# Optimization experiments

Measured on AMD Instinct MI355X. Metric: run time of the kernel, lower is better.

Reference implementation:

```python
import jax, jax.numpy as jnp
import numpy as np

B, SEQ, NVAR, DM, K = 2, 512, 64, 128, 2
SCALE = DM ** -0.5  # ScaledDotProductAttention scale, lsa=False so constant


def _period_branch(x4, Wel, bel, Wq, bq, Wk, bk, Wv, bv, Wo, bo, period):
    # x4: [B, DM(time), NVAR, DM(dim)] -- output of start_embed
    pad = (-DM) % period
    pn = (DM + pad) // period  # period_num
    xp = jnp.pad(x4, ((0, 0), (0, pad), (0, 0), (0, 0)))
    # torch .unfold(dim=1, size=period, step=period) -> [B, pn, NVAR, DM, period]
    xw = xp.reshape(B, pn, period, NVAR, DM).transpose(0, 1, 3, 4, 2)
    # emb_linear over the d_model (dim) axis
    xw = jnp.einsum('bqndl,ed->bqnel', xw, Wel) + bel[None, None, None, :, None]
    # -> [B, NVAR, dim, pn, period] then flatten to conv1d layout [bn, dim, L]
    X = xw.transpose(0, 2, 3, 1, 4).reshape(B * NVAR, DM, pn * period)
    # 1x1 Conv1d QKV projections over the channel (dim) axis
    q = jnp.einsum('bdl,ed->bel', X, Wq) + bq[None, :, None]
    k = jnp.einsum('bdl,ed->bel', X, Wk) + bk[None, :, None]
    v = jnp.einsum('bdl,ed->bel', X, Wv) + bv[None, :, None]
    q_s = q.reshape(B * NVAR, DM, pn, period).transpose(0, 1, 3, 2)  # [bn,dim,pl,pn]
    k_s = k.reshape(B * NVAR, DM, pn, period)                         # [bn,dim,pn,pl]
    v_s = v.reshape(B * NVAR, DM, pn, period).transpose(0, 1, 3, 2)  # [bn,dim,pl,pn]
    attn = jax.nn.softmax(jnp.einsum('bdip,bdpj->bdij', q_s, k_s) * SCALE, axis=-1)
    o = jnp.einsum('bdij,bdjp->bdip', attn, v_s)  # [bn, dim, period, pn]
    o = o.reshape(B * NVAR, DM, period * pn)[:, :, :DM]  # truncate to n_heads=DM
    return o @ Wo.T + bo  # to_out Linear(n_heads, n_heads), dropout eval-mode


def reference(x, W_emb, b_emb, W_start, b_start, Wel, bel, Wq, bq, Wk, bk, Wv, bv, Wo, bo, f1, f2):
    # inverted embedding: Linear(seq_len->d_model) over time, then permute -> [B, DM, NVAR]
    xe = (jnp.einsum('bsn,sd->bnd', x, W_emb) + b_emb).transpose(0, 2, 1)
    # FFT_for_Period amplitudes; top-k frequency indices f1,f2 are static (host-side in torch)
    amp = jnp.abs(jnp.fft.rfft(xe, axis=1)).mean(-1)  # [B, DM//2+1]
    pw = jax.nn.softmax(jnp.stack([amp[:, f1], amp[:, f2]], -1), axis=-1)  # [B, K]
    # start_embed: Linear(1 -> d_model) -> [B, DM, NVAR, DM]
    x4 = xe[..., None] * W_start + b_start
    outs = [_period_branch(x4, Wel, bel, Wq, bq, Wk, bk, Wv, bv, Wo, bo, DM // f)
            for f in (f1, f2)]
    res = jnp.stack(outs, -1)                      # [B*NVAR, DM, DM, K]
    pw_b = jnp.repeat(pw, NVAR, axis=0)            # [B*NVAR, K] (b-major order matches reshape)
    out = (res * pw_b[:, None, None, :]).sum(-1)
    return out.reshape(B, NVAR, DM, DM)


def setup_inputs() -> dict:
    key = jax.random.key(0)
    ks = jax.random.split(key, 16)
    s = 0.02
    d = {
        'x': jax.random.normal(ks[0], (B, SEQ, NVAR), jnp.float32),
        'W_emb': jax.random.normal(ks[1], (SEQ, DM), jnp.float32) * s,
        'b_emb': jax.random.normal(ks[2], (DM,), jnp.float32) * s,
        'W_start': jax.random.normal(ks[3], (DM,), jnp.float32) * s,
        'b_start': jax.random.normal(ks[4], (DM,), jnp.float32) * s,
        'Wel': jax.random.normal(ks[5], (DM, DM), jnp.float32) * s,
        'bel': jax.random.normal(ks[6], (DM,), jnp.float32) * s,
        'Wq': jax.random.normal(ks[7], (DM, DM), jnp.float32) * s,
        'bq': jax.random.normal(ks[8], (DM,), jnp.float32) * s,
        'Wk': jax.random.normal(ks[9], (DM, DM), jnp.float32) * s,
        'bk': jax.random.normal(ks[10], (DM,), jnp.float32) * s,
        'Wv': jax.random.normal(ks[11], (DM, DM), jnp.float32) * s,
        'bv': jax.random.normal(ks[12], (DM,), jnp.float32) * s,
        'Wo': jax.random.normal(ks[13], (DM, DM), jnp.float32) * s,
        'bo': jax.random.normal(ks[14], (DM,), jnp.float32) * s,
    }
    # host-side FFT period detection, mirroring torch's .detach().cpu().numpy() topk
    xe = np.einsum('bsn,sd->bnd', np.asarray(d['x']), np.asarray(d['W_emb'])) + np.asarray(d['b_emb'])
    xe = xe.transpose(0, 2, 1)  # [B, DM, NVAR]
    fl = np.abs(np.fft.rfft(xe, axis=1)).mean(0).mean(-1)
    fl[0] = 0.0
    top = np.argsort(-fl, kind='stable')[:K]
    d['f1'] = int(top[0])
    d['f2'] = int(top[1])
    return d
```

## Files before the change

kernel.cpp:

```cpp
#include <hip/hip_runtime.h>

#define DMD 128
#define NV 64
#define BB 2
#define SQ 512
#define NBN 128
#define ASCALE 0.08838834764831845f
#define L2E 1.4426950408889634f
#define LN2 0.6931471805599453f
#define CSC (ASCALE * L2E)

#define WS_XE  0
#define WS_VEC (WS_XE + NBN*DMD)
#define WS_OB  (WS_VEC + 9*DMD)
#define WS_AMP (WS_OB + NBN*DMD*DMD)
#define WS_G   (WS_AMP + NBN*2)
#define WS_MOM (WS_G + NBN*2*288)

__global__ __launch_bounds__(512) void k_xe(const float* __restrict__ x,
                                            const float* __restrict__ W_emb,
                                            const float* __restrict__ b_emb,
                                            const int* __restrict__ f1p,
                                            const int* __restrict__ f2p,
                                            const float* __restrict__ Wel, const float* __restrict__ bel,
                                            const float* __restrict__ W_start, const float* __restrict__ b_start,
                                            const float* __restrict__ Wq, const float* __restrict__ bq,
                                            const float* __restrict__ Wk, const float* __restrict__ bk,
                                            const float* __restrict__ Wv, const float* __restrict__ bv,
                                            float* __restrict__ ws) {
    int blk = blockIdx.x;
    int tid = threadIdx.x;
    __shared__ float xsh[SQ];
    __shared__ float part[3][DMD];
    __shared__ float red[2][7];
    __shared__ float xe_sh[DMD];
    __shared__ __align__(16) float A[DMD], C[DMD], BL[DMD];

    if (blk < NBN) {
        int bn = blk, b = bn >> 6, n = bn & 63;
        int t = tid & 127, sc = tid >> 7;
        int f1v = f1p[0], f2v = f2p[0];
        xsh[tid] = x[(b * SQ + tid) * NV + n];
        __syncthreads();
        float acc = 0.f;
        const float* W = W_emb + (sc * 128) * DMD + t;
#pragma unroll 8
        for (int s = 0; s < 128; ++s) acc = fmaf(xsh[sc * 128 + s], W[s * DMD], acc);
        if (sc) part[sc - 1][t] = acc;
        __syncthreads();
        if (sc == 0) {
            float r = acc + part[0][t] + part[1][t] + part[2][t] + b_emb[t];
            ws[WS_XE + bn * DMD + t] = r;
            xe_sh[t] = r;
            float angA = (float)((f1v * t) & 127) * 0.04908738521234052f;
            float angB = (float)((f2v * t) & 127) * 0.04908738521234052f;
            float v0 = r * cosf(angA), v1 = r * sinf(angA);
            float v2 = r * cosf(angB), v3 = r * sinf(angB);
            float v4 = r, v5 = r * r, v6 = v5 * r;
#pragma unroll
            for (int off = 32; off > 0; off >>= 1) {
                v0 += __shfl_xor(v0, off); v1 += __shfl_xor(v1, off);
                v2 += __shfl_xor(v2, off); v3 += __shfl_xor(v3, off);
                v4 += __shfl_xor(v4, off); v5 += __shfl_xor(v5, off);
                v6 += __shfl_xor(v6, off);
            }
            if ((tid & 63) == 0) {
                int w = tid >> 6;
                red[w][0] = v0; red[w][1] = v1; red[w][2] = v2; red[w][3] = v3;
                red[w][4] = v4; red[w][5] = v5; red[w][6] = v6;
            }
        }
        __syncthreads();
        if (tid == 0) {
            float re0 = red[0][0] + red[1][0], im0 = red[0][1] + red[1][1];
            float re1 = red[0][2] + red[1][2], im1 = red[0][3] + red[1][3];
            ws[WS_AMP + bn * 2 + 0] = sqrtf(re0 * re0 + im0 * im0);
            ws[WS_AMP + bn * 2 + 1] = sqrtf(re1 * re1 + im1 * im1);
            ws[WS_MOM + bn * 3 + 0] = red[0][4] + red[1][4];
            ws[WS_MOM + bn * 3 + 1] = red[0][5] + red[1][5];
            ws[WS_MOM + bn * 3 + 2] = red[0][6] + red[1][6];
        }
        {
            int br = tid >> 8;
            int entry = tid & 255;
            int f = br ? f2v : f1v;
            int P = DMD / f;
            if (P <= 16) {
                int pn = (DMD + P - 1) / P;
                int Prows = (DMD + pn - 1) / pn;
                int tot = Prows * P;
                if (entry < tot) {
                    int i = entry / P;
                    int j = entry - i * P;
                    float g = 0.f;
                    for (int p = 0; p < pn - 1; ++p)
                        g = fmaf(xe_sh[p * P + i], xe_sh[p * P + j], g);
                    ws[WS_G + (bn * 2 + br) * 288 + i * (P + 1) + j] = g;
                }
            }
        }
    } else {
        int e = tid;
        if (tid < 128) {
            float a = 0.f, c = 0.f;
            const float4* We4 = reinterpret_cast<const float4*>(Wel + e * DMD);
            const float4* Ws4 = reinterpret_cast<const float4*>(W_start);
            const float4* Bs4 = reinterpret_cast<const float4*>(b_start);
#pragma unroll 8
            for (int d4 = 0; d4 < 32; ++d4) {
                float4 w = We4[d4], s4 = Ws4[d4], t4 = Bs4[d4];
                a = fmaf(w.x, s4.x, fmaf(w.y, s4.y, fmaf(w.z, s4.z, fmaf(w.w, s4.w, a))));
                c = fmaf(w.x, t4.x, fmaf(w.y, t4.y, fmaf(w.z, t4.z, fmaf(w.w, t4.w, c))));
            }
            A[e] = a;
            C[e] = c + bel[e];
            BL[e] = bel[e];
        }
        __syncthreads();
        if (tid < 128) {
            float aq = 0, cq = 0, pq = 0, ak = 0, ck = 0, pk = 0, av = 0, cv = 0, pv = 0;
            const float4* Wq4 = reinterpret_cast<const float4*>(Wq + e * DMD);
            const float4* Wk4 = reinterpret_cast<const float4*>(Wk + e * DMD);
            const float4* Wv4 = reinterpret_cast<const float4*>(Wv + e * DMD);
            const float4* A4 = reinterpret_cast<const float4*>(A);
            const float4* C4 = reinterpret_cast<const float4*>(C);
            const float4* B4 = reinterpret_cast<const float4*>(BL);
#pragma unroll 4
            for (int d4 = 0; d4 < 32; ++d4) {
                float4 Ad = A4[d4], Cd = C4[d4], Bd = B4[d4];
                float4 wq = Wq4[d4], wk = Wk4[d4], wv = Wv4[d4];
                aq = fmaf(wq.x, Ad.x, fmaf(wq.y, Ad.y, fmaf(wq.z, Ad.z, fmaf(wq.w, Ad.w, aq))));
                cq = fmaf(wq.x, Cd.x, fmaf(wq.y, Cd.y, fmaf(wq.z, Cd.z, fmaf(wq.w, Cd.w, cq))));
                pq = fmaf(wq.x, Bd.x, fmaf(wq.y, Bd.y, fmaf(wq.z, Bd.z, fmaf(wq.w, Bd.w, pq))));
                ak = fmaf(wk.x, Ad.x, fmaf(wk.y, Ad.y, fmaf(wk.z, Ad.z, fmaf(wk.w, Ad.w, ak))));
                ck = fmaf(wk.x, Cd.x, fmaf(wk.y, Cd.y, fmaf(wk.z, Cd.z, fmaf(wk.w, Cd.w, ck))));
                pk = fmaf(wk.x, Bd.x, fmaf(wk.y, Bd.y, fmaf(wk.z, Bd.z, fmaf(wk.w, Bd.w, pk))));
                av = fmaf(wv.x, Ad.x, fmaf(wv.y, Ad.y, fmaf(wv.z, Ad.z, fmaf(wv.w, Ad.w, av))));
                cv = fmaf(wv.x, Cd.x, fmaf(wv.y, Cd.y, fmaf(wv.z, Cd.z, fmaf(wv.w, Cd.w, cv))));
                pv = fmaf(wv.x, Bd.x, fmaf(wv.y, Bd.y, fmaf(wv.z, Bd.z, fmaf(wv.w, Bd.w, pv))));
            }
            float* V = ws + WS_VEC;
            V[0 * DMD + e] = aq; V[1 * DMD + e] = cq + bq[e]; V[2 * DMD + e] = pq + bq[e];
            V[3 * DMD + e] = ak; V[4 * DMD + e] = ck + bk[e]; V[5 * DMD + e] = pk + bk[e];
            V[6 * DMD + e] = av; V[7 * DMD + e] = cv + bv[e]; V[8 * DMD + e] = pv + bv[e];
        }
    }
}


__device__ __forceinline__ void attn_rank1(const float (*Vsh)[4], const float* xs,
                                           float Sx, float Sxx, float Sxxx,
                                           float* __restrict__ ob, int rowbase, int tid) {
    float xi = xs[tid];
#pragma unroll
    for (int k = 0; k < 4; ++k) {
        float Aq = Vsh[0][k], Cq = Vsh[1][k], Ak = Vsh[3][k];
        float Av = Vsh[6][k], Cv = Vsh[7][k];
        float t = CSC * fmaf(xi, Aq, Cq) * Ak;
        float u = t * LN2;
        float hu = 0.5f * u;
        float l  = fmaf(u, fmaf(hu, Sxx,  Sx),  128.0f);
        float ax = fmaf(u, fmaf(hu, Sxxx, Sxx), Sx);
        ob[rowbase + k * DMD + tid] = fmaf(Av, ax / l, Cv);
    }
}

template<int PP, int NP, int EB>
__device__ __forceinline__ void attn_pow2(const float (*Vsh)[4],
                                          const float* xs, float* __restrict__ ob,
                                          int rowbase, int tid) {
    const int UH = PP / 4;
    int lane4 = tid & 3, i0 = tid >> 2, jb = lane4 * UH;

    float xq[NP][UH], U2[UH];
#pragma unroll
    for (int u = 0; u < UH; ++u) {
        int j = jb + u;
        float s = 0.f;
#pragma unroll
        for (int q = 0; q < NP; ++q) { float xv = xs[q * PP + j]; xq[q][u] = xv; s += xv; }
        U2[u] = s;
    }
    const int NREP = (PP == 64) ? 2 : 1;
#pragma unroll
    for (int rep = 0; rep < NREP; ++rep) {
        int i = i0 + rep * 32;
        float G2[UH];
#pragma unroll
        for (int u = 0; u < UH; ++u) G2[u] = 0.f;
#pragma unroll
        for (int q = 0; q < NP; ++q) {
            float xi = xs[q * PP + i];
#pragma unroll
            for (int u = 0; u < UH; ++u) G2[u] = fmaf(xi, xq[q][u], G2[u]);
        }
#pragma unroll
        for (int eg = 0; eg < 4; eg += EB) {
            float d1[EB], d2[EB], l[EB];
            float accq[NP][EB];
#pragma unroll
            for (int k = 0; k < EB; ++k) {
                float t = CSC * Vsh[3][eg + k];
                d1[k] = t * Vsh[0][eg + k];
                d2[k] = t * Vsh[1][eg + k];
                l[k] = 0.f;
#pragma unroll
                for (int q = 0; q < NP; ++q) accq[q][k] = 0.f;
            }
#pragma unroll
            for (int u = 0; u < UH; ++u) {
                float gg = G2[u], uu = U2[u];
                float ev[EB];
#pragma unroll
                for (int k = 0; k < EB; ++k) ev[k] = exp2f(fmaf(d1[k], gg, d2[k] * uu));
#pragma unroll
                for (int k = 0; k < EB; ++k) {
                    l[k] += ev[k];
#pragma unroll
                    for (int q = 0; q < NP; ++q) accq[q][k] = fmaf(ev[k], xq[q][u], accq[q][k]);
                }
            }
#pragma unroll
            for (int k = 0; k < EB; ++k) { l[k] += __shfl_xor(l[k], 1); l[k] += __shfl_xor(l[k], 2); }
#pragma unroll
            for (int q = 0; q < NP; ++q)
#pragma unroll
                for (int k = 0; k < EB; ++k) {
                    accq[q][k] += __shfl_xor(accq[q][k], 1);
                    accq[q][k] += __shfl_xor(accq[q][k], 2);
                }
            if (lane4 == 0) {
#pragma unroll
                for (int k = 0; k < EB; ++k) {
                    float li = 1.f / l[k];
                    float Av = Vsh[6][eg + k], Cv = Vsh[7][eg + k];
#pragma unroll
                    for (int q = 0; q < NP; ++q) {
                        ob[rowbase + (eg + k) * DMD + i * NP + q] = fmaf(Av, accq[q][k] * li, Cv);
                    }
                }
            }
        }
    }
}

template<int UB>
__device__ __forceinline__ void attn_small(
    int P, int pn, int r, int Prows,
    const float (*Vsh)[4], const float* xs, const float* U, const float* xt,
    const float* __restrict__ Gb, float* W, float* __restrict__ ob, int rowbase, int tid)
{
    int GP = P + 1;
    int tot = Prows * P;
    unsigned mP = (4096u + (unsigned)P - 1u) / (unsigned)P;
    unsigned mpn = (4096u + (unsigned)pn - 1u) / (unsigned)pn;

    bool v0 = (tid < tot);
    int i0 = (int)(((unsigned)tid * mP) >> 12);
    int j0 = tid - i0 * P;
    int wa0 = i0 * GP + j0;
    float g0 = Gb[wa0];
    bool A0 = (i0 < r), c0 = (j0 < r);
    float xtj0 = xt[j0], Uj0 = U[j0];
    float xti0 = A0 ? xt[i0] : 0.f;
    float Gx0 = (A0 && c0) ? fmaf(xti0, xtj0, g0) : g0;
    float Ux0 = (A0 && c0) ? Uj0 + xtj0 : Uj0;
    float Xw0 = (!A0 && c0) ? xtj0 : 0.f;
    float mw0 = c0 ? 1.f : 0.f;

    int idx1 = tid + 128;
    bool v1 = (idx1 < tot);
    int idx1c = v1 ? idx1 : 0;
    int i1 = (int)(((unsigned)idx1c * mP) >> 12);
    int j1 = idx1c - i1 * P;
    int wa1 = i1 * GP + j1;
    float g1 = Gb[wa1];
    bool A1 = (i1 < r), c1 = (j1 < r);
    float xtj1 = xt[j1], Uj1 = U[j1];
    float xti1 = A1 ? xt[i1] : 0.f;
    float Gx1 = (A1 && c1) ? fmaf(xti1, xtj1, g1) : g1;
    float Ux1 = (A1 && c1) ? Uj1 + xtj1 : Uj1;
    float Xw1 = (!A1 && c1) ? xtj1 : 0.f;
    float mw1 = c1 ? 1.f : 0.f;

    int i2 = (int)(((unsigned)tid * mpn) >> 12);
    int p2 = tid - i2 * pn;
    bool lastp = (p2 == pn - 1);
    int row2 = i2 * GP;
    float xsr[UB];
#pragma unroll
    for (int j = 0; j < UB; ++j) {
        int idx = p2 * P + j;
        xsr[j] = (j < P && idx < DMD) ? xs[idx] : 0.f;
    }

    float s[4][2];
#pragma unroll
    for (int ec = 0; ec < 4; ++ec) {
        float Aq = Vsh[0][ec], Cq = Vsh[1][ec], Pq = Vsh[2][ec];
        float Ak = Vsh[3][ec], Ck = Vsh[4][ec], Pk = Vsh[5][ec];
        float t = CSC * Ak;
        float d1 = t * Aq, d2 = t * Cq, d3 = t * Pq;
        float ckpk = CSC * (Ck - Pk);
        float aS0 = A0 ? fmaf(Aq, xti0, Cq) : Pq;
        s[ec][0] = fmaf(d1, Gx0, fmaf(d2, Ux0, fmaf(d3, Xw0, (ckpk * aS0) * mw0)));
        float aS1 = A1 ? fmaf(Aq, xti1, Cq) : Pq;
        s[ec][1] = fmaf(d1, Gx1, fmaf(d2, Ux1, fmaf(d3, Xw1, (ckpk * aS1) * mw1)));
    }
#pragma unroll
    for (int ec = 0; ec < 4; ++ec) { s[ec][0] = exp2f(s[ec][0]); s[ec][1] = exp2f(s[ec][1]); }
#pragma unroll
    for (int ec = 0; ec < 4; ++ec) {
        if (v0) W[ec * 288 + wa0] = s[ec][0];
        if (v1) W[ec * 288 + wa1] = s[ec][1];
    }
    __syncthreads();

#pragma unroll
    for (int ec = 0; ec < 4; ++ec) {
        float Av = Vsh[6][ec], Cv = Vsh[7][ec], Pv = Vsh[8][ec];
        float l = 0.f, wr = 0.f, ax = 0.f;
#pragma unroll
        for (int j = 0; j < UB; ++j) {
            float w = W[ec * 288 + row2 + ((j < P) ? j : 0)];
            w = (j < P) ? w : 0.f;
            l += w;
            wr += (j < r) ? w : 0.f;
            ax = fmaf(w, xsr[j], ax);
        }
        float li = 1.f / l;
        float o;
        if (lastp) { float sl = wr * li; o = fmaf(Av, ax * li, fmaf(Cv, sl, Pv * (1.f - sl))); }
        else       o = fmaf(Av, ax * li, Cv);
        ob[rowbase + ec * DMD + tid] = o;
    }
}

template<int UH, int NP>
__device__ __forceinline__ void attn_midA(
    int P, int pn, int r, int Prows,
    const float (*Vsh)[4], const float* xs, const float* U,
    const float* xt, float* __restrict__ ob, int rowbase, int tid)
{
    int lane4 = tid & 3;
    int i0 = tid >> 2;
    int jb = lane4 * UH;

    float Ur[UH], xtr[UH], xq0[UH], xq1[UH];
#pragma unroll
    for (int u = 0; u < UH; ++u) {
        int j = jb + u, jc = (j < P) ? j : 0;
        Ur[u] = U[jc];
        xtr[u] = xt[jc];
        xq0[u] = (j < DMD) ? xs[j] : 0.f;
        int i1x = P + j;
        xq1[u] = (i1x < DMD) ? xs[i1x] : 0.f;
    }
    int nrep = (Prows > 32) ? 2 : 1;
    for (int rep = 0; rep < nrep; ++rep) {
        int i = i0 + rep * 32;
        bool rowact = (i < Prows);
        int ic = rowact ? i : 0;
        float xtic = xt[ic];
        bool rowvalid = (ic < r);
        float g[UH];
#pragma unroll
        for (int u = 0; u < UH; ++u) g[u] = 0.f;
        for (int p = 0; p < pn - 1; ++p) {
            float xi = xs[p * P + ic];
#pragma unroll
            for (int u = 0; u < UH; ++u) {
                int j = jb + u, jc = (j < P) ? j : 0;
                g[u] = fmaf(xi, xs[p * P + jc], g[u]);
            }
        }
        for (int ec = 0; ec < 4; ++ec) {
            float Aq = Vsh[0][ec], Cq = Vsh[1][ec], Pq = Vsh[2][ec];
            float Ak = Vsh[3][ec], Ck = Vsh[4][ec], Pk = Vsh[5][ec];
            float Av = Vsh[6][ec], Cv = Vsh[7][ec], Pv = Vsh[8][ec];
            float c1 = CSC * Aq * Ak, c3 = CSC * Cq * Ak;
            float asi = CSC * (rowvalid ? fmaf(xtic, Aq, Cq) : Pq);

            float l0 = 0.f, l1 = 0.f, w0 = 0.f, w1 = 0.f;
            float accq[NP];
#pragma unroll
            for (int q = 0; q < NP; ++q) accq[q] = 0.f;
#pragma unroll
            for (int u = 0; u < UH; ++u) {
                int j = jb + u;
                float bK = (j < r) ? fmaf(xtr[u], Ak, Ck) : Pk;
                float S = fmaf(asi, bK, fmaf(c3, Ur[u], c1 * g[u]));
                float ev = exp2f(S);
                ev = (j < P) ? ev : 0.f;
                if (u & 1) l1 += ev; else l0 += ev;
                float evr = (j < r) ? ev : 0.f;
                if (u & 1) w1 += evr; else w0 += evr;
                accq[0] = fmaf(ev, xq0[u], accq[0]);
                if (NP >= 2) accq[1] = fmaf(ev, xq1[u], accq[1]);
#pragma unroll
                for (int q = 2; q < NP; ++q) {
                    int idx = q * P + j;
                    float xv = (idx < DMD) ? xs[idx] : 0.f;
                    accq[q] = fmaf(ev, xv, accq[q]);
                }
            }
            float l = l0 + l1, wr = w0 + w1;
            l += __shfl_xor(l, 1);  l += __shfl_xor(l, 2);
            wr += __shfl_xor(wr, 1); wr += __shfl_xor(wr, 2);
#pragma unroll
            for (int q = 0; q < NP; ++q) {
                if (q < pn) {
                    accq[q] += __shfl_xor(accq[q], 1);
                    accq[q] += __shfl_xor(accq[q], 2);
                }
            }
            if (lane4 == 0 && rowact) {
                float li = 1.f / l;
#pragma unroll
                for (int q = 0; q < NP; ++q) {
                    if (q < pn) {
                        int mo = i * pn + q;
                        if (mo < DMD) {
                            float o;
                            if (q == pn - 1) {
                                float sl = wr * li;
                                o = fmaf(Av, accq[q] * li, fmaf(Cv, sl, Pv * (1.f - sl)));
                            } else {
                                o = fmaf(Av, accq[q] * li, Cv);
                            }
                            ob[rowbase + ec * DMD + mo] = o;
                        }
                    }
                }
            }
        }
    }
}

__global__ __launch_bounds__(128) void k_attn(const int* __restrict__ f1p,
                                              const int* __restrict__ f2p,
                                              float* __restrict__ ws,
                                              float* __restrict__ outb) {
    int bn = blockIdx.y;
    int e0 = blockIdx.x * 4;
    int br = blockIdx.z;
    int tid = threadIdx.x;

    __shared__ float xs[DMD], U[64], xt[64];
    __shared__ float Vsh[9][4];
    __shared__ float W[4 * 288];

    xs[tid] = ws[WS_XE + bn * DMD + tid];
    if (tid < 36) Vsh[tid >> 2][tid & 3] = ws[WS_VEC + (tid >> 2) * DMD + e0 + (tid & 3)];
    int f = br ? f2p[0] : f1p[0];
    float* ob = br ? outb : (ws + WS_OB);
    const float* Gb = ws + WS_G + (bn * 2 + br) * 288;
    int rowbase = (bn * DMD + e0) * DMD;

    float Sx = 0.f, Sxx = 0.f, Sxxx = 0.f;
    if (f == 1) {
        const float* M = ws + WS_MOM + bn * 3;
        Sx = M[0]; Sxx = M[1]; Sxxx = M[2];
    }
    __syncthreads();

    int P = DMD / f;
    int pn = (DMD + P - 1) / P;
    int r = DMD - (pn - 1) * P;
    int Prows = (DMD + pn - 1) / pn;

    if (P == DMD) {
        attn_rank1(Vsh, xs, Sx, Sxx, Sxxx, ob, rowbase, tid);
        return;
    }
    if (tid < P) {
        float s = 0.f;
        for (int p = 0; p < pn - 1; ++p) s += xs[p * P + tid];
        U[tid] = s;
        xt[tid] = (tid < r) ? xs[(pn - 1) * P + tid] : 0.f;
    }
    __syncthreads();

    if (P <= 4)       attn_small<4>(P, pn, r, Prows, Vsh, xs, U, xt, Gb, W, ob, rowbase, tid);
    else if (P <= 8)  attn_small<8>(P, pn, r, Prows, Vsh, xs, U, xt, Gb, W, ob, rowbase, tid);
    else if (P <= 16) attn_small<16>(P, pn, r, Prows, Vsh, xs, U, xt, Gb, W, ob, rowbase, tid);
    else if (P == 64) attn_pow2<64, 2, 2>(Vsh, xs, ob, rowbase, tid);
    else if (P == 32) attn_pow2<32, 4, 4>(Vsh, xs, ob, rowbase, tid);
    else if (P > 32)  attn_midA<16, 4>(P, pn, r, Prows, Vsh, xs, U, xt, ob, rowbase, tid);
    else              attn_midA<8, 8>(P, pn, r, Prows, Vsh, xs, U, xt, ob, rowbase, tid);
}

__global__ __launch_bounds__(256) void k_out(const float* __restrict__ Wo,
                                             const float* __restrict__ bo,
                                             const float* __restrict__ ws,
                                             float* __restrict__ out) {
    int blk = blockIdx.x;
    int bn = blk >> 2;
    int e0 = (blk & 3) * 32;
    int b = bn >> 6;
    int tid = threadIdx.x;
    __shared__ __align__(16) float WTc[32 * 132];
    __shared__ __align__(16) float oT[32][36];
    __shared__ float pwsh[2];
    int hg = tid & 31, eg = tid >> 5, h0 = hg * 4;

    if (tid < 64) {
        float a0 = ws[WS_AMP + (b * NV + tid) * 2 + 0];
        float a1 = ws[WS_AMP + (b * NV + tid) * 2 + 1];
#pragma unroll
        for (int off = 32; off > 0; off >>= 1) {
            a0 += __shfl_down(a0, off);
            a1 += __shfl_down(a1, off);
        }
        if (tid == 0) {
            a0 *= (1.0f / NV); a1 *= (1.0f / NV);
            float m = fmaxf(a0, a1);
            float e0v = expf(a0 - m), e1v = expf(a1 - m);
            float inv = 1.0f / (e0v + e1v);
            pwsh[0] = e0v * inv;
            pwsh[1] = e1v * inv;
        }
    }
    __syncthreads();
    float pw0 = pwsh[0], pw1 = pwsh[1];

    float acc[4][4];
#pragma unroll
    for (int c = 0; c < 4; ++c)
#pragma unroll
        for (int d = 0; d < 4; ++d) acc[c][d] = 0.f;

    for (int mc = 0; mc < 4; ++mc) {
        int m0 = mc * 32;
        __syncthreads();
        for (int idx = tid; idx < 4096; idx += 256) {
            int h = idx >> 5, mm = idx & 31;
            WTc[mm * 132 + h] = Wo[h * DMD + m0 + mm];
        }
        for (int idx = tid; idx < 1024; idx += 256) {
            int e = idx >> 5, mm = idx & 31;
            int gi = (bn * DMD + e0 + e) * DMD + m0 + mm;
            oT[mm][e] = fmaf(pw0, ws[WS_OB + gi], pw1 * out[gi]);
        }
        __syncthreads();
#pragma unroll 4
        for (int mm = 0; mm < 32; ++mm) {
            const float4 wv = *reinterpret_cast<const float4*>(&WTc[mm * 132 + h0]);
            const float4 q0 = *reinterpret_cast<const float4*>(&oT[mm][eg * 4]);
            float ae[4] = {q0.x, q0.y, q0.z, q0.w};
#pragma unroll
            for (int el = 0; el < 4; ++el) {
                float a = ae[el];
                acc[el][0] = fmaf(a, wv.x, acc[el][0]);
                acc[el][1] = fmaf(a, wv.y, acc[el][1]);
                acc[el][2] = fmaf(a, wv.z, acc[el][2]);
                acc[el][3] = fmaf(a, wv.w, acc[el][3]);
            }
        }
    }
    const float4 bov = *reinterpret_cast<const float4*>(&bo[h0]);
#pragma unroll
    for (int el = 0; el < 4; ++el) {
        float4 res = { acc[el][0] + bov.x, acc[el][1] + bov.y,
                       acc[el][2] + bov.z, acc[el][3] + bov.w };
        int e = e0 + eg * 4 + el;
        *reinterpret_cast<float4*>(&out[(bn * DMD + e) * DMD + h0]) = res;
    }
}

extern "C" void kernel_launch(void* const* d_in, const int* in_sizes, int n_in,
                              void* d_out, int out_size, void* d_ws, size_t ws_size,
                              hipStream_t stream) {
    const float* x       = (const float*)d_in[0];
    const float* W_emb   = (const float*)d_in[1];
    const float* b_emb   = (const float*)d_in[2];
    const float* W_start = (const float*)d_in[3];
    const float* b_start = (const float*)d_in[4];
    const float* Wel     = (const float*)d_in[5];
    const float* bel     = (const float*)d_in[6];
    const float* Wq      = (const float*)d_in[7];
    const float* bq      = (const float*)d_in[8];
    const float* Wk      = (const float*)d_in[9];
    const float* bk      = (const float*)d_in[10];
    const float* Wv      = (const float*)d_in[11];
    const float* bv      = (const float*)d_in[12];
    const float* Wo      = (const float*)d_in[13];
    const float* bo      = (const float*)d_in[14];
    const int*   f1p     = (const int*)d_in[15];
    const int*   f2p     = (const int*)d_in[16];
    float* ws  = (float*)d_ws;
    float* out = (float*)d_out;

    k_xe<<<NBN + 1, 512, 0, stream>>>(x, W_emb, b_emb, f1p, f2p,
                                      Wel, bel, W_start, b_start,
                                      Wq, bq, Wk, bk, Wv, bv, ws);
    k_attn<<<dim3(32, NBN, 2), 128, 0, stream>>>(f1p, f2p, ws, out);
    k_out<<<512, 256, 0, stream>>>(Wo, bo, ws, out);
}
```

Baseline: 74.56 us.

## Fuse branch combination and output projection into attention kernel

The attention kernel now computes both period branches in one block, accumulating the period-weighted sum into shared memory. It then applies the Wo projection directly, using a transposed Wo prepared in the first kernel, so the separate output kernel goes away. This removes the 8 MB round trip of per-branch outputs through global memory and the reread in the output kernel. In exchange it adds a tiny kernel for the period weights, serialises the two branches inside each block (halving the grid), and precomputes softmax row sums in attn_small.

```diff
diff --git a/kernel.cpp b/kernel.cpp
--- a/kernel.cpp
+++ b/kernel.cpp
@@ -12,10 +12,11 @@
 
 #define WS_XE  0
 #define WS_VEC (WS_XE + NBN*DMD)
-#define WS_OB  (WS_VEC + 9*DMD)
-#define WS_AMP (WS_OB + NBN*DMD*DMD)
+#define WS_PW  (WS_VEC + 9*DMD)
+#define WS_AMP (WS_PW + 4)
 #define WS_G   (WS_AMP + NBN*2)
 #define WS_MOM (WS_G + NBN*2*288)
+#define WS_WOT (WS_MOM + NBN*3)
 
 __global__ __launch_bounds__(512) void k_xe(const float* __restrict__ x,
                                             const float* __restrict__ W_emb,
@@ -27,6 +28,7 @@
                                             const float* __restrict__ Wq, const float* __restrict__ bq,
                                             const float* __restrict__ Wk, const float* __restrict__ bk,
                                             const float* __restrict__ Wv, const float* __restrict__ bv,
+                                            const float* __restrict__ Wo,
                                             float* __restrict__ ws) {
     int blk = blockIdx.x;
     int tid = threadIdx.x;
@@ -100,6 +102,10 @@
             }
         }
     } else {
+        for (int idx = tid; idx < DMD * DMD; idx += 512) {
+            int m = idx >> 7, h = idx & 127;
+            ws[WS_WOT + idx] = Wo[h * DMD + m];
+        }
         int e = tid;
         if (tid < 128) {
             float a = 0.f, c = 0.f;
@@ -147,10 +153,35 @@
     }
 }
 
+__global__ __launch_bounds__(128) void k_pw(float* __restrict__ ws) {
+    int tid = threadIdx.x;
+    int b = tid >> 6, n = tid & 63;
+    float a0 = ws[WS_AMP + (b * NV + n) * 2 + 0];
+    float a1 = ws[WS_AMP + (b * NV + n) * 2 + 1];
+#pragma unroll
+    for (int off = 32; off > 0; off >>= 1) {
+        a0 += __shfl_down(a0, off);
+        a1 += __shfl_down(a1, off);
+    }
+    if (n == 0) {
+        a0 *= (1.0f / NV); a1 *= (1.0f / NV);
+        float m = fmaxf(a0, a1);
+        float e0 = expf(a0 - m), e1 = expf(a1 - m);
+        float inv = 1.0f / (e0 + e1);
+        ws[WS_PW + b * 2 + 0] = e0 * inv;
+        ws[WS_PW + b * 2 + 1] = e1 * inv;
+    }
+}
+
+
+__device__ __forceinline__ void osh_put(float* Osh, int pos, float v, float pwv, int br) {
+    if (br == 0) Osh[pos] = pwv * v;
+    else         Osh[pos] += pwv * v;
+}
 
 __device__ __forceinline__ void attn_rank1(const float (*Vsh)[4], const float* xs,
                                            float Sx, float Sxx, float Sxxx,
-                                           float* __restrict__ ob, int rowbase, int tid) {
+                                           float* Osh, float pwv, int br, int tid) {
     float xi = xs[tid];
 #pragma unroll
     for (int k = 0; k < 4; ++k) {
@@ -161,14 +192,13 @@
         float hu = 0.5f * u;
         float l  = fmaf(u, fmaf(hu, Sxx,  Sx),  128.0f);
         float ax = fmaf(u, fmaf(hu, Sxxx, Sxx), Sx);
-        ob[rowbase + k * DMD + tid] = fmaf(Av, ax / l, Cv);
+        osh_put(Osh, k * 128 + tid, fmaf(Av, ax / l, Cv), pwv, br);
     }
 }
 
 template<int PP, int NP, int EB>
-__device__ __forceinline__ void attn_pow2(const float (*Vsh)[4],
-                                          const float* xs, float* __restrict__ ob,
-                                          int rowbase, int tid) {
+__device__ __forceinline__ void attn_pow2(const float (*Vsh)[4], const float* xs,
+                                          float* Osh, float pwv, int br, int tid) {
     const int UH = PP / 4;
     int lane4 = tid & 3, i0 = tid >> 2, jb = lane4 * UH;
 
@@ -235,9 +265,9 @@
                     float li = 1.f / l[k];
                     float Av = Vsh[6][eg + k], Cv = Vsh[7][eg + k];
 #pragma unroll
-                    for (int q = 0; q < NP; ++q) {
-                        ob[rowbase + (eg + k) * DMD + i * NP + q] = fmaf(Av, accq[q][k] * li, Cv);
-                    }
+                    for (int q = 0; q < NP; ++q)
+                        osh_put(Osh, (eg + k) * 128 + i * NP + q,
+                                fmaf(Av, accq[q][k] * li, Cv), pwv, br);
                 }
             }
         }
@@ -248,7 +278,8 @@
 __device__ __forceinline__ void attn_small(
     int P, int pn, int r, int Prows,
     const float (*Vsh)[4], const float* xs, const float* U, const float* xt,
-    const float* __restrict__ Gb, float* W, float* __restrict__ ob, int rowbase, int tid)
+    const float* __restrict__ Gb, float* W, float* Li, float* Sl,
+    float* Osh, float pwv, int br, int tid)
 {
     int GP = P + 1;
     int tot = Prows * P;
@@ -316,23 +347,40 @@
     }
     __syncthreads();
 
+    if (tid < Prows) {
+        int row = tid * GP;
+#pragma unroll
+        for (int ec = 0; ec < 4; ++ec) {
+            float l = 0.f, wr = 0.f;
+#pragma unroll
+            for (int j = 0; j < UB; ++j) {
+                if (j < P) {
+                    float w = W[ec * 288 + row + j];
+                    l += w;
+                    wr += (j < r) ? w : 0.f;
+                }
+            }
+            float li = 1.f / l;
+            Li[ec * 128 + tid] = li;
+            Sl[ec * 128 + tid] = wr * li;
+        }
+    }
+    __syncthreads();
+
 #pragma unroll
     for (int ec = 0; ec < 4; ++ec) {
         float Av = Vsh[6][ec], Cv = Vsh[7][ec], Pv = Vsh[8][ec];
-        float l = 0.f, wr = 0.f, ax = 0.f;
+        float ax = 0.f;
 #pragma unroll
         for (int j = 0; j < UB; ++j) {
             float w = W[ec * 288 + row2 + ((j < P) ? j : 0)];
-            w = (j < P) ? w : 0.f;
-            l += w;
-            wr += (j < r) ? w : 0.f;
             ax = fmaf(w, xsr[j], ax);
         }
-        float li = 1.f / l;
+        float li = Li[ec * 128 + i2];
         float o;
-        if (lastp) { float sl = wr * li; o = fmaf(Av, ax * li, fmaf(Cv, sl, Pv * (1.f - sl))); }
+        if (lastp) { float sl = Sl[ec * 128 + i2]; o = fmaf(Av, ax * li, fmaf(Cv, sl, Pv * (1.f - sl))); }
         else       o = fmaf(Av, ax * li, Cv);
-        ob[rowbase + ec * DMD + tid] = o;
+        osh_put(Osh, ec * 128 + tid, o, pwv, br);
     }
 }
 
@@ -340,7 +388,7 @@
 __device__ __forceinline__ void attn_midA(
     int P, int pn, int r, int Prows,
     const float (*Vsh)[4], const float* xs, const float* U,
-    const float* xt, float* __restrict__ ob, int rowbase, int tid)
+    const float* xt, float* Osh, float pwv, int br, int tid)
 {
     int lane4 = tid & 3;
     int i0 = tid >> 2;
@@ -428,7 +476,7 @@
                             } else {
                                 o = fmaf(Av, accq[q] * li, Cv);
                             }
-                            ob[rowbase + ec * DMD + mo] = o;
+                            osh_put(Osh, ec * 128 + mo, o, pwv, br);
                         }
                     }
                 }
@@ -439,133 +487,84 @@
 
 __global__ __launch_bounds__(128) void k_attn(const int* __restrict__ f1p,
                                               const int* __restrict__ f2p,
+                                              const float* __restrict__ bo,
                                               float* __restrict__ ws,
-                                              float* __restrict__ outb) {
+                                              float* __restrict__ out) {
     int bn = blockIdx.y;
+    int b = bn >> 6;
     int e0 = blockIdx.x * 4;
-    int br = blockIdx.z;
     int tid = threadIdx.x;
 
     __shared__ float xs[DMD], U[64], xt[64];
     __shared__ float Vsh[9][4];
     __shared__ float W[4 * 288];
+    __shared__ float Li[4 * 128], Sl[4 * 128];
+    __shared__ float Osh[4 * 128];
 
     xs[tid] = ws[WS_XE + bn * DMD + tid];
     if (tid < 36) Vsh[tid >> 2][tid & 3] = ws[WS_VEC + (tid >> 2) * DMD + e0 + (tid & 3)];
-    int f = br ? f2p[0] : f1p[0];
-    float* ob = br ? outb : (ws + WS_OB);
-    const float* Gb = ws + WS_G + (bn * 2 + br) * 288;
-    int rowbase = (bn * DMD + e0) * DMD;
-
-    float Sx = 0.f, Sxx = 0.f, Sxxx = 0.f;
-    if (f == 1) {
-        const float* M = ws + WS_MOM + bn * 3;
-        Sx = M[0]; Sxx = M[1]; Sxxx = M[2];
-    }
+    int f1v = f1p[0], f2v = f2p[0];
+    float pw0 = ws[WS_PW + b * 2 + 0];
+    float pw1 = ws[WS_PW + b * 2 + 1];
     __syncthreads();
 
-    int P = DMD / f;
-    int pn = (DMD + P - 1) / P;
-    int r = DMD - (pn - 1) * P;
-    int Prows = (DMD + pn - 1) / pn;
-
-    if (P == DMD) {
-        attn_rank1(Vsh, xs, Sx, Sxx, Sxxx, ob, rowbase, tid);
-        return;
-    }
-    if (tid < P) {
-        float s = 0.f;
-        for (int p = 0; p < pn - 1; ++p) s += xs[p * P + tid];
-        U[tid] = s;
-        xt[tid] = (tid < r) ? xs[(pn - 1) * P + tid] : 0.f;
+    for (int br = 0; br < 2; ++br) {
+        int f = br ? f2v : f1v;
+        float pwv = br ? pw1 : pw0;
+        const float* Gb = ws + WS_G + (bn * 2 + br) * 288;
+        int P = DMD / f;
+        int pn = (DMD + P - 1) / P;
+        int r = DMD - (pn - 1) * P;
+        int Prows = (DMD + pn - 1) / pn;
+
+        if (br == 1) __syncthreads();
+
+        if (P == DMD) {
+            const float* M = ws + WS_MOM + bn * 3;
+            attn_rank1(Vsh, xs, M[0], M[1], M[2], Osh, pwv, br, tid);
+            continue;
+        }
+        if (tid < P) {
+            float s = 0.f;
+            for (int p = 0; p < pn - 1; ++p) s += xs[p * P + tid];
+            U[tid] = s;
+            xt[tid] = (tid < r) ? xs[(pn - 1) * P + tid] : 0.f;
+        }
+        __syncthreads();
+
+        if (P <= 4)       attn_small<4>(P, pn, r, Prows, Vsh, xs, U, xt, Gb, W, Li, Sl, Osh, pwv, br, tid);
+        else if (P <= 8)  attn_small<8>(P, pn, r, Prows, Vsh, xs, U, xt, Gb, W, Li, Sl, Osh, pwv, br, tid);
+        else if (P <= 16) attn_small<16>(P, pn, r, Prows, Vsh, xs, U, xt, Gb, W, Li, Sl, Osh, pwv, br, tid);
+        else if (P == 64) attn_pow2<64, 2, 2>(Vsh, xs, Osh, pwv, br, tid);
+        else if (P == 32) attn_pow2<32, 4, 4>(Vsh, xs, Osh, pwv, br, tid);
+        else if (P > 32)  attn_midA<16, 4>(P, pn, r, Prows, Vsh, xs, U, xt, Osh, pwv, br, tid);
+        else              attn_midA<8, 8>(P, pn, r, Prows, Vsh, xs, U, xt, Osh, pwv, br, tid);
     }
     __syncthreads();
 
-    if (P <= 4)       attn_small<4>(P, pn, r, Prows, Vsh, xs, U, xt, Gb, W, ob, rowbase, tid);
-    else if (P <= 8)  attn_small<8>(P, pn, r, Prows, Vsh, xs, U, xt, Gb, W, ob, rowbase, tid);
-    else if (P <= 16) attn_small<16>(P, pn, r, Prows, Vsh, xs, U, xt, Gb, W, ob, rowbase, tid);
-    else if (P == 64) attn_pow2<64, 2, 2>(Vsh, xs, ob, rowbase, tid);
-    else if (P == 32) attn_pow2<32, 4, 4>(Vsh, xs, ob, rowbase, tid);
-    else if (P > 32)  attn_midA<16, 4>(P, pn, r, Prows, Vsh, xs, U, xt, ob, rowbase, tid);
-    else              attn_midA<8, 8>(P, pn, r, Prows, Vsh, xs, U, xt, ob, rowbase, tid);
-}
-
-__global__ __launch_bounds__(256) void k_out(const float* __restrict__ Wo,
-                                             const float* __restrict__ bo,
-                                             const float* __restrict__ ws,
-                                             float* __restrict__ out) {
-    int blk = blockIdx.x;
-    int bn = blk >> 2;
-    int e0 = (blk & 3) * 32;
-    int b = bn >> 6;
-    int tid = threadIdx.x;
-    __shared__ __align__(16) float WTc[32 * 132];
-    __shared__ __align__(16) float oT[32][36];
-    __shared__ float pwsh[2];
-    int hg = tid & 31, eg = tid >> 5, h0 = hg * 4;
-
-    if (tid < 64) {
-        float a0 = ws[WS_AMP + (b * NV + tid) * 2 + 0];
-        float a1 = ws[WS_AMP + (b * NV + tid) * 2 + 1];
-#pragma unroll
-        for (int off = 32; off > 0; off >>= 1) {
-            a0 += __shfl_down(a0, off);
-            a1 += __shfl_down(a1, off);
-        }
-        if (tid == 0) {
-            a0 *= (1.0f / NV); a1 *= (1.0f / NV);
-            float m = fmaxf(a0, a1);
-            float e0v = expf(a0 - m), e1v = expf(a1 - m);
-            float inv = 1.0f / (e0v + e1v);
-            pwsh[0] = e0v * inv;
-            pwsh[1] = e1v * inv;
-        }
-    }
-    __syncthreads();
-    float pw0 = pwsh[0], pw1 = pwsh[1];
-
-    float acc[4][4];
-#pragma unroll
-    for (int c = 0; c < 4; ++c)
-#pragma unroll
-        for (int d = 0; d < 4; ++d) acc[c][d] = 0.f;
-
-    for (int mc = 0; mc < 4; ++mc) {
-        int m0 = mc * 32;
-        __syncthreads();
-        for (int idx = tid; idx < 4096; idx += 256) {
-            int h = idx >> 5, mm = idx & 31;
-            WTc[mm * 132 + h] = Wo[h * DMD + m0 + mm];
-        }
-        for (int idx = tid; idx < 1024; idx += 256) {
-            int e = idx >> 5, mm = idx & 31;
-            int gi = (bn * DMD + e0 + e) * DMD + m0 + mm;
-            oT[mm][e] = fmaf(pw0, ws[WS_OB + gi], pw1 * out[gi]);
-        }
-        __syncthreads();
-#pragma unroll 4
-        for (int mm = 0; mm < 32; ++mm) {
-            const float4 wv = *reinterpret_cast<const float4*>(&WTc[mm * 132 + h0]);
-            const float4 q0 = *reinterpret_cast<const float4*>(&oT[mm][eg * 4]);
-            float ae[4] = {q0.x, q0.y, q0.z, q0.w};
-#pragma unroll
-            for (int el = 0; el < 4; ++el) {
-                float a = ae[el];
-                acc[el][0] = fmaf(a, wv.x, acc[el][0]);
-                acc[el][1] = fmaf(a, wv.y, acc[el][1]);
-                acc[el][2] = fmaf(a, wv.z, acc[el][2]);
-                acc[el][3] = fmaf(a, wv.w, acc[el][3]);
-            }
-        }
-    }
-    const float4 bov = *reinterpret_cast<const float4*>(&bo[h0]);
-#pragma unroll
-    for (int el = 0; el < 4; ++el) {
-        float4 res = { acc[el][0] + bov.x, acc[el][1] + bov.y,
-                       acc[el][2] + bov.z, acc[el][3] + bov.w };
-        int e = e0 + eg * 4 + el;
-        *reinterpret_cast<float4*>(&out[(bn * DMD + e) * DMD + h0]) = res;
-    }
+    const float* WoT = ws + WS_WOT;
+    float a0 = 0.f, a1 = 0.f, a2 = 0.f, a3 = 0.f;
+#pragma unroll 8
+    for (int mo4 = 0; mo4 < DMD; mo4 += 4) {
+        float w0 = WoT[(mo4 + 0) * DMD + tid];
+        float w1 = WoT[(mo4 + 1) * DMD + tid];
+        float w2 = WoT[(mo4 + 2) * DMD + tid];
+        float w3 = WoT[(mo4 + 3) * DMD + tid];
+        const float4 o0 = *reinterpret_cast<const float4*>(&Osh[0 * 128 + mo4]);
+        const float4 o1 = *reinterpret_cast<const float4*>(&Osh[1 * 128 + mo4]);
+        const float4 o2 = *reinterpret_cast<const float4*>(&Osh[2 * 128 + mo4]);
+        const float4 o3 = *reinterpret_cast<const float4*>(&Osh[3 * 128 + mo4]);
+        a0 = fmaf(o0.x, w0, fmaf(o0.y, w1, fmaf(o0.z, w2, fmaf(o0.w, w3, a0))));
+        a1 = fmaf(o1.x, w0, fmaf(o1.y, w1, fmaf(o1.z, w2, fmaf(o1.w, w3, a1))));
+        a2 = fmaf(o2.x, w0, fmaf(o2.y, w1, fmaf(o2.z, w2, fmaf(o2.w, w3, a2))));
+        a3 = fmaf(o3.x, w0, fmaf(o3.y, w1, fmaf(o3.z, w2, fmaf(o3.w, w3, a3))));
+    }
+    float bov = bo[tid];
+    int obase = (bn * DMD + e0) * DMD + tid;
+    out[obase + 0 * DMD] = a0 + bov;
+    out[obase + 1 * DMD] = a1 + bov;
+    out[obase + 2 * DMD] = a2 + bov;
+    out[obase + 3 * DMD] = a3 + bov;
 }
 
 extern "C" void kernel_launch(void* const* d_in, const int* in_sizes, int n_in,
@@ -593,7 +592,7 @@
 
     k_xe<<<NBN + 1, 512, 0, stream>>>(x, W_emb, b_emb, f1p, f2p,
                                       Wel, bel, W_start, b_start,
-                                      Wq, bq, Wk, bk, Wv, bv, ws);
-    k_attn<<<dim3(32, NBN, 2), 128, 0, stream>>>(f1p, f2p, ws, out);
-    k_out<<<512, 256, 0, stream>>>(Wo, bo, ws, out);
-}
+                                      Wq, bq, Wk, bk, Wv, bv, Wo, ws);
+    k_pw<<<1, 128, 0, stream>>>(ws);
+    k_attn<<<dim3(32, NBN), 128, 0, stream>>>(f1p, f2p, bo, ws, out);
+}
```

New measurement: 75.86 us. Within noise of the previous version (+1.7%).
